# Performance work log

Hardware: AMD Instinct MI355X
Metric: run time of the kernel (lower is better)

## Reference

```python
import jax, jax.numpy as jnp
import numpy as np

N_NODES = 20000
N_EDGES = 640000
HIDDEN = 256
HEADS = 8
HEAD_DIM = HIDDEN // HEADS
VOCAB = 119
N_FEATS = 9


def setup_inputs() -> dict:
    key = jax.random.key(0)
    ks = jax.random.split(key, 12)
    X = jax.random.randint(ks[0], (N_NODES, N_FEATS), 0, VOCAB)
    edge_row = jnp.sort(jax.random.randint(ks[1], (N_EDGES,), 0, N_NODES))
    edge_col = jax.random.randint(ks[2], (N_EDGES,), 0, N_NODES)
    s = 0.05  # init scale to keep activations sane
    emb_tables = jax.random.normal(ks[3], (N_FEATS, VOCAB, HIDDEN), jnp.float32) * s
    q_w = jax.random.normal(ks[4], (HIDDEN, HIDDEN), jnp.float32) * s
    q_b = jax.random.normal(ks[5], (HIDDEN,), jnp.float32) * s
    k_w = jax.random.normal(ks[6], (HIDDEN, HIDDEN), jnp.float32) * s
    k_b = jax.random.normal(ks[7], (HIDDEN,), jnp.float32) * s
    v_w = jax.random.normal(ks[8], (HIDDEN, HIDDEN), jnp.float32) * s
    v_b = jax.random.normal(ks[9], (HIDDEN,), jnp.float32) * s
    o_w = jax.random.normal(ks[10], (HIDDEN, HIDDEN), jnp.float32) * s
    o_b = jax.random.normal(ks[11], (HIDDEN,), jnp.float32) * s
    return dict(X=X, edge_row=edge_row, edge_col=edge_col, emb_tables=emb_tables,
                q_w=q_w, q_b=q_b, k_w=k_w, k_b=k_b, v_w=v_w, v_b=v_b, o_w=o_w, o_b=o_b)


def reference(X, edge_row, edge_col, emb_tables, q_w, q_b, k_w, k_b, v_w, v_b, o_w, o_b):
    N = X.shape[0]
    # AtomEncoder: sum of per-feature embeddings -> [N, HIDDEN]
    feat_idx = jnp.arange(N_FEATS)[None, :]  # [1, 9]
    h = emb_tables[feat_idx, X].sum(axis=1)  # [N, 9, H] -> [N, H]
    # q/k/v projections (torch Linear: y = x W^T + b), split into heads
    q = (h @ q_w.T + q_b).reshape(N, HEADS, HEAD_DIM) * (HEAD_DIM ** -0.5)
    k = (h @ k_w.T + k_b).reshape(N, HEADS, HEAD_DIM)
    v = (h @ v_w.T + v_b).reshape(N, HEADS, HEAD_DIM)
    # SDDMM: per-edge, per-head scores
    s = jnp.einsum('ehd,ehd->eh', q[edge_row], k[edge_col])  # [E, HEADS]
    # sparse row-wise softmax (over each node's outgoing-edge neighbors)
    m = jax.ops.segment_max(s, edge_row, num_segments=N)
    e = jnp.exp(s - m[edge_row])
    z = jax.ops.segment_sum(e, edge_row, num_segments=N)
    attn = e / z[edge_row]  # [E, HEADS]
    # SPMM: weighted aggregation of neighbor values
    out = jax.ops.segment_sum(attn[:, :, None] * v[edge_col], edge_row, num_segments=N)
    return out.reshape(N, HIDDEN) @ o_w.T + o_b
```

## Files before the change

### kernel.cpp

```cpp
#include <hip/hip_runtime.h>
#include <hip/hip_bf16.h>

#define N_NODES 20000
#define N_EDGES 640000
#define HIDDEN 256
#define HEADS 8
#define HEAD_DIM 32
#define N_FEATS 9
#define VOCAB 119

typedef __hip_bfloat16 bf16;
typedef __attribute__((ext_vector_type(8))) short short8;
typedef __attribute__((ext_vector_type(4))) float f32x4;
typedef __attribute__((ext_vector_type(2))) float f32x2;

__device__ __forceinline__ ushort f2u(float x) { union { ushort u; bf16 b; } c; c.b = __float2bfloat16(x); return c.u; }

__device__ __forceinline__ f32x2 pk_fma(f32x2 a, f32x2 b, f32x2 c) {
    f32x2 d;
    asm("v_pk_fma_f32 %0, %1, %2, %3" : "=v"(d) : "v"(a), "v"(b), "v"(c));
    return d;
}
__device__ __forceinline__ f32x2 pk_add(f32x2 a, f32x2 b) {
    f32x2 d;
    asm("v_pk_add_f32 %0, %1, %2" : "=v"(d) : "v"(a), "v"(b));
    return d;
}

template <int CTRL>
__device__ __forceinline__ float dpp_xor(float v) {
    return __int_as_float(__builtin_amdgcn_update_dpp(
        0, __float_as_int(v), CTRL, 0xf, 0xf, true));
}

__device__ __forceinline__ float fast_exp2(float x) {
#if __has_builtin(__builtin_amdgcn_exp2f)
    return __builtin_amdgcn_exp2f(x);
#else
    return exp2f(x);
#endif
}

#if __has_builtin(__builtin_amdgcn_fdot2_f32_bf16)
typedef __attribute__((ext_vector_type(2))) __bf16 bf16x2_t;
__device__ __forceinline__ float dot2bf(uint a, uint b, float c) {
    return __builtin_amdgcn_fdot2_f32_bf16(__builtin_bit_cast(bf16x2_t, a),
                                           __builtin_bit_cast(bf16x2_t, b), c, false);
}
#else
__device__ __forceinline__ float dot2bf(uint a, uint b, float c) {
    return c + __uint_as_float(a << 16) * __uint_as_float(b << 16)
             + __uint_as_float(a & 0xffff0000u) * __uint_as_float(b & 0xffff0000u);
}
#endif

__global__ void k_pre(const int* __restrict__ X, const float* __restrict__ emb,
                      bf16* __restrict__ h,
                      const float* __restrict__ qw, const float* __restrict__ kw,
                      const float* __restrict__ vw, const float* __restrict__ ow,
                      const float* __restrict__ qb, const float* __restrict__ kb,
                      const float* __restrict__ vb,
                      bf16* __restrict__ wqkv, bf16* __restrict__ wo,
                      float* __restrict__ qkvb,
                      const int* __restrict__ erow, int* __restrict__ row_ptr) {
    int b = blockIdx.x;
    if (b < 5000) {
        int tid = b * 256 + threadIdx.x;
        int n = tid >> 6;
        int c4 = (tid & 63) * 4;
        float4 a = make_float4(0.f, 0.f, 0.f, 0.f);
#pragma unroll
        for (int f = 0; f < N_FEATS; ++f) {
            int idx = X[n * N_FEATS + f];
            float4 e = *(const float4*)(emb + ((size_t)(f * VOCAB + idx)) * HIDDEN + c4);
            a.x += e.x; a.y += e.y; a.z += e.z; a.w += e.w;
        }
        ushort4 o = make_ushort4(f2u(a.x), f2u(a.y), f2u(a.z), f2u(a.w));
        *(ushort4*)((ushort*)h + (size_t)n * HIDDEN + c4) = o;
    } else if (b < 6027) {
        int i = (b - 5000) * 256 + threadIdx.x;
        if (i < 196608) {
            const float* s = i < 65536 ? qw : i < 131072 ? kw : vw;
            wqkv[i] = __float2bfloat16(s[i & 65535]);
        } else if (i < 262144) {
            wo[i - 196608] = __float2bfloat16(ow[i - 196608]);
        } else if (i < 262912) {
            int j = i - 262144;
            const float* s = j < 256 ? qb : j < 512 ? kb : vb;
            qkvb[j] = s[j & 255];
        }
    } else {
        int n = (b - 6027) * 256 + threadIdx.x;
        if (n > N_NODES) return;
        int lo = 0, hi = N_EDGES;
        while (lo < hi) {
            int mid = (lo + hi) >> 1;
            if (erow[mid] < n) lo = mid + 1; else hi = mid;
        }
        row_ptr[n] = lo;
    }
}

template <int MODE, bool GUARD, int TM>
__device__ __forceinline__ void gemm_core(const bf16* __restrict__ A,
                                          const bf16* __restrict__ W,
                                          const float* __restrict__ bias,
                                          void* __restrict__ Y0, void* __restrict__ Y1,
                                          float s_q, int n0, int d0) {
    constexpr int RI = TM / 32;
    __shared__ short As[TM * 72];
    __shared__ short Bs[128 * 72];
    int t = threadIdx.x;
    int lane = t & 63, w = t >> 6;
    int wr = (w >> 1) * (TM / 2), wc = (w & 1) * 64;
    int lr = lane & 15, quad = lane >> 4;

    f32x4 acc[RI][4] = {};
    short8 ra[RI], rb[4];
    int srowA[RI], skoA[RI], srowB[4], skoB[4];
#pragma unroll
    for (int it = 0; it < RI; ++it) { int c = t + 256 * it; srowA[it] = c >> 3; skoA[it] = (c & 7) * 8; }
#pragma unroll
    for (int it = 0; it < 4; ++it) { int c = t + 256 * it; srowB[it] = c >> 3; skoB[it] = (c & 7) * 8; }

#pragma unroll
    for (int it = 0; it < RI; ++it) {
        int n = n0 + srowA[it];
        short8 av = {};
        if (!GUARD || n < N_NODES) av = *(const short8*)(A + (size_t)n * HIDDEN + skoA[it]);
        ra[it] = av;
    }
#pragma unroll
    for (int it = 0; it < 4; ++it)
        rb[it] = *(const short8*)(W + (size_t)(d0 + srowB[it]) * HIDDEN + skoB[it]);
#pragma unroll
    for (int it = 0; it < RI; ++it) *(short8*)(&As[srowA[it] * 72 + skoA[it]]) = ra[it];
#pragma unroll
    for (int it = 0; it < 4; ++it)  *(short8*)(&Bs[srowB[it] * 72 + skoB[it]]) = rb[it];
    __syncthreads();

    for (int k0 = 64; k0 < 256; k0 += 64) {
#pragma unroll
        for (int it = 0; it < RI; ++it) {
            int n = n0 + srowA[it];
            short8 av = {};
            if (!GUARD || n < N_NODES) av = *(const short8*)(A + (size_t)n * HIDDEN + k0 + skoA[it]);
            ra[it] = av;
        }
#pragma unroll
        for (int it = 0; it < 4; ++it)
            rb[it] = *(const short8*)(W + (size_t)(d0 + srowB[it]) * HIDDEN + k0 + skoB[it]);
        {
            short8 af[RI][2], bfr[4][2];
#pragma unroll
            for (int i = 0; i < RI; ++i)
#pragma unroll
                for (int kk = 0; kk < 2; ++kk)
                    af[i][kk] = *(short8*)(&As[(wr + i * 16 + lr) * 72 + kk * 32 + quad * 8]);
#pragma unroll
            for (int j = 0; j < 4; ++j)
#pragma unroll
                for (int kk = 0; kk < 2; ++kk)
                    bfr[j][kk] = *(short8*)(&Bs[(wc + j * 16 + lr) * 72 + kk * 32 + quad * 8]);
#pragma unroll
            for (int kk = 0; kk < 2; ++kk)
#pragma unroll
                for (int i = 0; i < RI; ++i)
#pragma unroll
                    for (int j = 0; j < 4; ++j)
                        acc[i][j] = __builtin_amdgcn_mfma_f32_16x16x32_bf16(
                            af[i][kk], bfr[j][kk], acc[i][j], 0, 0, 0);
        }
        __syncthreads();
#pragma unroll
        for (int it = 0; it < RI; ++it) *(short8*)(&As[srowA[it] * 72 + skoA[it]]) = ra[it];
#pragma unroll
        for (int it = 0; it < 4; ++it)  *(short8*)(&Bs[srowB[it] * 72 + skoB[it]]) = rb[it];
        __syncthreads();
    }
    {
        short8 af[RI][2], bfr[4][2];
#pragma unroll
        for (int i = 0; i < RI; ++i)
#pragma unroll
            for (int kk = 0; kk < 2; ++kk)
                af[i][kk] = *(short8*)(&As[(wr + i * 16 + lr) * 72 + kk * 32 + quad * 8]);
#pragma unroll
        for (int j = 0; j < 4; ++j)
#pragma unroll
            for (int kk = 0; kk < 2; ++kk)
                bfr[j][kk] = *(short8*)(&Bs[(wc + j * 16 + lr) * 72 + kk * 32 + quad * 8]);
#pragma unroll
        for (int kk = 0; kk < 2; ++kk)
#pragma unroll
            for (int i = 0; i < RI; ++i)
#pragma unroll
                for (int j = 0; j < 4; ++j)
                    acc[i][j] = __builtin_amdgcn_mfma_f32_16x16x32_bf16(
                        af[i][kk], bfr[j][kk], acc[i][j], 0, 0, 0);
    }

#pragma unroll
    for (int j = 0; j < 4; ++j) {
        int dbase = d0 + wc + j * 16;
        float bj = bias[dbase + lr];
        if constexpr (MODE == 0) {
            float sc = (dbase < 256) ? s_q : 1.f;
            ushort* dst; int stride;
            if (dbase < 256) {
                dst = (ushort*)Y0 + (size_t)(dbase >> 6) * N_NODES * 64 + (dbase & 63) + lr;
                stride = 64;
            } else if (dbase < 512) {
                int e = dbase - 256;
                dst = (ushort*)Y1 + (size_t)(e >> 6) * N_NODES * 128 + (e & 63) + lr;
                stride = 128;
            } else {
                int e = dbase - 512;
                dst = (ushort*)Y1 + (size_t)(e >> 6) * N_NODES * 128 + 64 + (e & 63) + lr;
                stride = 128;
            }
#pragma unroll
            for (int i = 0; i < RI; ++i)
#pragma unroll
                for (int r = 0; r < 4; ++r) {
                    int n = n0 + wr + i * 16 + quad * 4 + r;
                    if (GUARD && n >= N_NODES) continue;
                    dst[(size_t)n * stride] = f2u((acc[i][j][r] + bj) * sc);
                }
        } else {
            float* dst = (float*)Y0 + dbase + lr;
#pragma unroll
            for (int i = 0; i < RI; ++i)
#pragma unroll
                for (int r = 0; r < 4; ++r) {
                    int n = n0 + wr + i * 16 + quad * 4 + r;
                    if (GUARD && n >= N_NODES) continue;
                    dst[(size_t)n * HIDDEN] = acc[i][j][r] + bj;
                }
        }
    }
}

__global__ __launch_bounds__(256, 2) void k_gemm_qkv(
    const bf16* __restrict__ A, const bf16* __restrict__ wqkv,
    const float* __restrict__ qkvb, ushort* __restrict__ qhp,
    ushort* __restrict__ kvhp, float qscale) {
    int n0 = blockIdx.x * 128;
    if (n0 + 128 <= N_NODES)
        gemm_core<0, false, 128>(A, wqkv, qkvb, qhp, kvhp, qscale, n0, blockIdx.y * 128);
    else
        gemm_core<0, true, 128>(A, wqkv, qkvb, qhp, kvhp, qscale, n0, blockIdx.y * 128);
}

__global__ __launch_bounds__(256, 4) void k_gemm_o(
    const bf16* __restrict__ A, const bf16* __restrict__ W,
    const float* __restrict__ bias, float* __restrict__ Y) {
    int n0 = blockIdx.x * 64;
    if (n0 + 64 <= N_NODES)
        gemm_core<1, false, 64>(A, W, bias, Y, nullptr, 1.f, n0, blockIdx.y * 128);
    else
        gemm_core<1, true, 64>(A, W, bias, Y, nullptr, 1.f, n0, blockIdx.y * 128);
}


template <int NIT>
__device__ __forceinline__ void pv_accum(const uint4* vv, const float* pb,
                                         f32x2& av0, f32x2& av1, f32x2& av2v, f32x2& av3) {
#pragma unroll
    for (int it = 0; it < NIT; ++it) {
        f32x2 pp; pp.x = pb[it]; pp.y = pb[it];
        f32x2 vf0, vf1, vf2, vf3;
        vf0.x = __uint_as_float(vv[it].x << 16); vf0.y = __uint_as_float(vv[it].x & 0xffff0000u);
        vf1.x = __uint_as_float(vv[it].y << 16); vf1.y = __uint_as_float(vv[it].y & 0xffff0000u);
        vf2.x = __uint_as_float(vv[it].z << 16); vf2.y = __uint_as_float(vv[it].z & 0xffff0000u);
        vf3.x = __uint_as_float(vv[it].w << 16); vf3.y = __uint_as_float(vv[it].w & 0xffff0000u);
        av0  = pk_fma(vf0, pp, av0);
        av1  = pk_fma(vf1, pp, av1);
        av2v = pk_fma(vf2, pp, av2v);
        av3  = pk_fma(vf3, pp, av3);
    }
}

__device__ __forceinline__ void attn_combine(int lane, int d8, float z,
                                             f32x2 av0, f32x2 av1, f32x2 av2v, f32x2 av3,
                                             ushort* __restrict__ orow) {
    bool b3 = (lane & 8) != 0, b4 = (lane & 16) != 0, b5 = (lane & 32) != 0;
    f32x2 sd0 = b3 ? av0 : av2v;
    f32x2 sd1 = b3 ? av1 : av3;
    f32x2 r0, r1;
    r0.x = dpp_xor<0x128>(sd0.x); r0.y = dpp_xor<0x128>(sd0.y);
    r1.x = dpp_xor<0x128>(sd1.x); r1.y = dpp_xor<0x128>(sd1.y);
    f32x2 t0 = pk_add(b3 ? av2v : av0, r0);
    f32x2 t1 = pk_add(b3 ? av3  : av1, r1);
    f32x2 sdu = b4 ? t0 : t1;
    f32x2 ru; ru.x = __shfl_xor(sdu.x, 16); ru.y = __shfl_xor(sdu.y, 16);
    f32x2 u = pk_add(b4 ? t1 : t0, ru);
    float sw = b5 ? u.x : u.y;
    float rw = __shfl_xor(sw, 32);
    float w = (b5 ? u.y : u.x) + rw;
    int dim = d8 * 8 + ((lane >> 3) & 1) * 4 + ((lane >> 4) & 1) * 2 + ((lane >> 5) & 1);
    orow[dim] = f2u(w * (1.f / z));
}

__global__ __launch_bounds__(256, 4) void k_attn(
    const int* __restrict__ row_ptr, const int* __restrict__ col,
    const ushort* __restrict__ qhp, const ushort* __restrict__ kvhp,
    bf16* __restrict__ agg) {
    int b = blockIdx.x;
    int x = b & 7;
    int hp = x & 3;
    int wave = __builtin_amdgcn_readfirstlane((int)(threadIdx.x >> 6));
    int n = (b >> 3) * 8 + (x >> 2) * 4 + wave;
    int lane = threadIdx.x & 63;
    int my = lane >> 3;
    int d8 = lane & 7;

    int start = row_ptr[n];
    int deg = row_ptr[n + 1] - start;

    ushort* orow = (ushort*)agg + (size_t)n * HIDDEN + hp * 64;
    if (deg == 0) {
        if (lane < 8) { uint4 zo = {}; *(uint4*)(orow + lane * 8) = zo; }
        return;
    }

    const ushort* qrow = qhp + ((size_t)hp * N_NODES + n) * 64;
    const ushort* kvbase = kvhp + (size_t)hp * N_NODES * 128;
    const int* cb = col + start;

    if (deg <= 32) {
        int e = lane >> 1, h = lane & 1;
        int c_e = cb[min(e, deg - 1)];
        const ushort* kp = kvbase + (((size_t)(uint)c_e) << 7) + (uint)h * 32;
        const ushort* qp = qrow + (uint)h * 32;

        int cv[4]; uint4 vv[4];
#pragma unroll
        for (int it = 0; it < 4; ++it) cv[it] = __shfl(c_e, (it * 8 + my) * 2);
#pragma unroll
        for (int it = 0; it < 4; ++it)
            vv[it] = *(const uint4*)(kvbase + (((size_t)(uint)cv[it]) << 7) + 64 + (uint)d8 * 8);

        uint4 kk[4], qq[4];
#pragma unroll
        for (int i = 0; i < 4; ++i) kk[i] = *(const uint4*)(kp + i * 8);
#pragma unroll
        for (int i = 0; i < 4; ++i) qq[i] = *(const uint4*)(qp + i * 8);

        float c0 = dot2bf(kk[0].x, qq[0].x, 0.f);
        float c1 = dot2bf(kk[0].y, qq[0].y, 0.f);
        float c2 = dot2bf(kk[0].z, qq[0].z, 0.f);
        float c3 = dot2bf(kk[0].w, qq[0].w, 0.f);
#pragma unroll
        for (int i = 1; i < 4; ++i) {
            c0 = dot2bf(kk[i].x, qq[i].x, c0);
            c1 = dot2bf(kk[i].y, qq[i].y, c1);
            c2 = dot2bf(kk[i].z, qq[i].z, c2);
            c3 = dot2bf(kk[i].w, qq[i].w, c3);
        }
        float s = (c0 + c1) + (c2 + c3);
        float p = (e < deg) ? fast_exp2(s) : 0.f;

        float z = p;
        z += dpp_xor<0x4E>(z);
        z += dpp_xor<0x124>(z);
        z += dpp_xor<0x128>(z);
        z += __shfl_xor(z, 16);
        z += __shfl_xor(z, 32);
        float zo = __shfl_xor(z, 1);
        float zf = (h == (d8 >> 2)) ? z : zo;

        float pb[4];
#pragma unroll
        for (int it = 0; it < 4; ++it)
            pb[it] = __shfl(p, (it * 8 + my) * 2 + (d8 >> 2));

        f32x2 av0 = {0.f, 0.f}, av1 = {0.f, 0.f}, av2v = {0.f, 0.f}, av3 = {0.f, 0.f};
        pv_accum<4>(vv, pb, av0, av1, av2v, av3);
        attn_combine(lane, d8, zf, av0, av1, av2v, av3, orow);

    } else if (deg <= 64) {
        int c_all = cb[min(lane, deg - 1)];
        const ushort* kp = kvbase + (((size_t)(uint)c_all) << 7);

        int cv[8]; uint4 vv[8];
#pragma unroll
        for (int it = 0; it < 8; ++it) cv[it] = __shfl(c_all, it * 8 + my);
#pragma unroll
        for (int it = 0; it < 8; ++it)
            vv[it] = *(const uint4*)(kvbase + (((size_t)(uint)cv[it]) << 7) + 64 + (uint)d8 * 8);

        uint4 kk[8], qv[8];
#pragma unroll
        for (int i = 0; i < 8; ++i) kk[i] = *(const uint4*)(kp + i * 8);
#pragma unroll
        for (int i = 0; i < 8; ++i) qv[i] = *(const uint4*)(qrow + i * 8);

        float a0 = dot2bf(kk[0].x, qv[0].x, 0.f);
        float a1 = dot2bf(kk[0].y, qv[0].y, 0.f);
        float a2 = dot2bf(kk[0].z, qv[0].z, 0.f);
        float a3 = dot2bf(kk[0].w, qv[0].w, 0.f);
        float b0 = dot2bf(kk[4].x, qv[4].x, 0.f);
        float b1 = dot2bf(kk[4].y, qv[4].y, 0.f);
        float b2 = dot2bf(kk[4].z, qv[4].z, 0.f);
        float b3s = dot2bf(kk[4].w, qv[4].w, 0.f);
#pragma unroll
        for (int i = 1; i < 4; ++i) {
            a0 = dot2bf(kk[i].x, qv[i].x, a0);
            a1 = dot2bf(kk[i].y, qv[i].y, a1);
            a2 = dot2bf(kk[i].z, qv[i].z, a2);
            a3 = dot2bf(kk[i].w, qv[i].w, a3);
            b0 = dot2bf(kk[4 + i].x, qv[4 + i].x, b0);
            b1 = dot2bf(kk[4 + i].y, qv[4 + i].y, b1);
            b2 = dot2bf(kk[4 + i].z, qv[4 + i].z, b2);
            b3s = dot2bf(kk[4 + i].w, qv[4 + i].w, b3s);
        }
        float sA = (a0 + a1) + (a2 + a3);
        float sB = (b0 + b1) + (b2 + b3s);
        bool val = lane < deg;
        float pA = val ? fast_exp2(sA) : 0.f;
        float pB = val ? fast_exp2(sB) : 0.f;

        f32x2 zz; zz.x = pA; zz.y = pB;
        {
            f32x2 r;
            r.x = dpp_xor<0xB1>(zz.x);  r.y = dpp_xor<0xB1>(zz.y);  zz = pk_add(zz, r);
            r.x = dpp_xor<0x4E>(zz.x);  r.y = dpp_xor<0x4E>(zz.y);  zz = pk_add(zz, r);
            r.x = dpp_xor<0x124>(zz.x); r.y = dpp_xor<0x124>(zz.y); zz = pk_add(zz, r);
            r.x = dpp_xor<0x128>(zz.x); r.y = dpp_xor<0x128>(zz.y); zz = pk_add(zz, r);
            r.x = __shfl_xor(zz.x, 16); r.y = __shfl_xor(zz.y, 16); zz = pk_add(zz, r);
            r.x = __shfl_xor(zz.x, 32); r.y = __shfl_xor(zz.y, 32); zz = pk_add(zz, r);
        }
        float zf = (d8 < 4) ? zz.x : zz.y;

        bool hB = (d8 >= 4);
        float pb[8];
#pragma unroll
        for (int it = 0; it < 8; ++it) {
            float pa_ = __shfl(pA, it * 8 + my);
            float pb_ = __shfl(pB, it * 8 + my);
            pb[it] = hB ? pb_ : pa_;
        }

        f32x2 av0 = {0.f, 0.f}, av1 = {0.f, 0.f}, av2v = {0.f, 0.f}, av3 = {0.f, 0.f};
        pv_accum<8>(vv, pb, av0, av1, av2v, av3);
        attn_combine(lane, d8, zf, av0, av1, av2v, av3, orow);

    } else {
        uint4 qu = *(const uint4*)(qrow + d8 * 8);
        float z = 0.f;
        f32x2 av0 = {0.f, 0.f}, av1 = {0.f, 0.f}, av2v = {0.f, 0.f}, av3 = {0.f, 0.f};
        for (int i = 0; i < deg; i += 8) {
            int idx = i + my;
            int cidx = idx < deg ? idx : deg - 1;
            int c = cb[cidx];
            const ushort* kp = kvbase + (((size_t)(uint)c) << 7) + (uint)d8 * 8;
            uint4 ku = *(const uint4*)(kp);
            uint4 vu = *(const uint4*)(kp + 64);
            float s = dot2bf(ku.x, qu.x, 0.f);
            s = dot2bf(ku.y, qu.y, s);
            s = dot2bf(ku.z, qu.z, s);
            s = dot2bf(ku.w, qu.w, s);
            s += dpp_xor<0xB1>(s);
            s += dpp_xor<0x4E>(s);
            float p = (idx < deg) ? fast_exp2(s) : 0.f;
            z += p;
            f32x2 pp; pp.x = p; pp.y = p;
            f32x2 vf0, vf1, vf2, vf3;
            vf0.x = __uint_as_float(vu.x << 16); vf0.y = __uint_as_float(vu.x & 0xffff0000u);
            vf1.x = __uint_as_float(vu.y << 16); vf1.y = __uint_as_float(vu.y & 0xffff0000u);
            vf2.x = __uint_as_float(vu.z << 16); vf2.y = __uint_as_float(vu.z & 0xffff0000u);
            vf3.x = __uint_as_float(vu.w << 16); vf3.y = __uint_as_float(vu.w & 0xffff0000u);
            av0  = pk_fma(vf0, pp, av0);
            av1  = pk_fma(vf1, pp, av1);
            av2v = pk_fma(vf2, pp, av2v);
            av3  = pk_fma(vf3, pp, av3);
        }
        z += dpp_xor<0x128>(z);
        z += __shfl_xor(z, 16);
        z += __shfl_xor(z, 32);
        attn_combine(lane, d8, z, av0, av1, av2v, av3, orow);
    }
}

extern "C" void kernel_launch(void* const* d_in, const int* in_sizes, int n_in,
                              void* d_out, int out_size, void* d_ws, size_t ws_size,
                              hipStream_t stream) {
    const int*   X    = (const int*)d_in[0];
    const int*   erow = (const int*)d_in[1];
    const int*   ecol = (const int*)d_in[2];
    const float* emb  = (const float*)d_in[3];
    const float* q_w  = (const float*)d_in[4];
    const float* q_b  = (const float*)d_in[5];
    const float* k_w  = (const float*)d_in[6];
    const float* k_b  = (const float*)d_in[7];
    const float* v_w  = (const float*)d_in[8];
    const float* v_b  = (const float*)d_in[9];
    const float* o_w  = (const float*)d_in[10];
    const float* o_b  = (const float*)d_in[11];
    float* out = (float*)d_out;

    char* ws = (char*)d_ws;
    bf16*   h    = (bf16*)(ws);
    bf16*   agg  = (bf16*)(ws);
    ushort* qhp  = (ushort*)(ws + 10240000);
    ushort* kvhp = (ushort*)(ws + 20480000);
    bf16*   wqkv = (bf16*)(ws + 40960000);
    bf16*   wo   = (bf16*)(ws + 41353216);
    float*  qkvb = (float*)(ws + 41484288);
    int* row_ptr = (int*)(ws + 41487360);

    k_pre<<<6106, 256, 0, stream>>>(X, emb, h, q_w, k_w, v_w, o_w,
                                    q_b, k_b, v_b, wqkv, wo, qkvb, erow, row_ptr);

    const float qscale = 0.25503486121587466f;
    dim3 gqkv((N_NODES + 127) / 128, 768 / 128);
    k_gemm_qkv<<<gqkv, 256, 0, stream>>>(h, wqkv, qkvb, qhp, kvhp, qscale);

    k_attn<<<N_NODES, 256, 0, stream>>>(row_ptr, ecol, qhp, kvhp, agg);

    dim3 go((N_NODES + 63) / 64, HIDDEN / 128);
    k_gemm_o<<<go, 256, 0, stream>>>(agg, wo, o_b, out);
}
```

Measured before the change: 190.0 us.

## Unify small-degree attention paths into edge-per-8-lane layout with scheduling fence

Replaces the two small-degree branches (where one or two lanes computed a whole head-pair score from many strided K and Q loads) with a shared templated path. In it each group of 8 lanes owns one edge, each lane loads only one 16-byte K chunk, and a single Q chunk is reused across edges. Scores are reduced with DPP, so the later per-edge probability shuffles disappear and the softmax sum is taken per lane. A sched_barrier keeps all gather loads issued before any compute, which aims to improve memory-level parallelism and cut register use on Q loads. The cost is extra cross-lane reductions per edge and more rigid instruction scheduling.

```diff
diff --git a/kernel.cpp b/kernel.cpp
--- a/kernel.cpp
+++ b/kernel.cpp
@@ -39,6 +39,10 @@
 #else
     return exp2f(x);
 #endif
+}
+
+__device__ __forceinline__ void sched_fence() {
+    __builtin_amdgcn_sched_barrier(0);
 }
 
 #if __has_builtin(__builtin_amdgcn_fdot2_f32_bf16)
@@ -302,6 +306,54 @@
     orow[dim] = f2u(w * (1.f / z));
 }
 
+template <int NIT>
+__device__ __forceinline__ void attn_dense(const int* __restrict__ cb, int deg,
+                                           int lane, int my, int d8,
+                                           const ushort* __restrict__ qrow,
+                                           const ushort* __restrict__ kvbase,
+                                           ushort* __restrict__ orow) {
+    int degm8 = deg - my;
+    int c_all = cb[min(lane, deg - 1)];
+    uint d8b = (uint)d8 * 8;
+
+    int cc[NIT];
+#pragma unroll
+    for (int it = 0; it < NIT; ++it) cc[it] = __shfl(c_all, it * 8 + my);
+
+    uint4 qu = *(const uint4*)(qrow + d8b);
+    uint4 kk[NIT], vv[NIT];
+#pragma unroll
+    for (int it = 0; it < NIT; ++it)
+        kk[it] = *(const uint4*)(kvbase + (((size_t)(uint)cc[it]) << 7) + d8b);
+#pragma unroll
+    for (int it = 0; it < NIT; ++it)
+        vv[it] = *(const uint4*)(kvbase + (((size_t)(uint)cc[it]) << 7) + 64 + d8b);
+
+    sched_fence();
+
+    float z = 0.f;
+    float pb[NIT];
+#pragma unroll
+    for (int it = 0; it < NIT; ++it) {
+        float s = dot2bf(kk[it].x, qu.x, 0.f);
+        s = dot2bf(kk[it].y, qu.y, s);
+        s = dot2bf(kk[it].z, qu.z, s);
+        s = dot2bf(kk[it].w, qu.w, s);
+        s += dpp_xor<0xB1>(s);
+        s += dpp_xor<0x4E>(s);
+        float p = (it * 8 < degm8) ? fast_exp2(s) : 0.f;
+        z += p;
+        pb[it] = p;
+    }
+    z += dpp_xor<0x128>(z);
+    z += __shfl_xor(z, 16);
+    z += __shfl_xor(z, 32);
+
+    f32x2 av0 = {0.f, 0.f}, av1 = {0.f, 0.f}, av2v = {0.f, 0.f}, av3 = {0.f, 0.f};
+    pv_accum<NIT>(vv, pb, av0, av1, av2v, av3);
+    attn_combine(lane, d8, z, av0, av1, av2v, av3, orow);
+}
+
 __global__ __launch_bounds__(256, 4) void k_attn(
     const int* __restrict__ row_ptr, const int* __restrict__ col,
     const ushort* __restrict__ qhp, const ushort* __restrict__ kvhp,
@@ -329,123 +381,9 @@
     const int* cb = col + start;
 
     if (deg <= 32) {
-        int e = lane >> 1, h = lane & 1;
-        int c_e = cb[min(e, deg - 1)];
-        const ushort* kp = kvbase + (((size_t)(uint)c_e) << 7) + (uint)h * 32;
-        const ushort* qp = qrow + (uint)h * 32;
-
-        int cv[4]; uint4 vv[4];
-#pragma unroll
-        for (int it = 0; it < 4; ++it) cv[it] = __shfl(c_e, (it * 8 + my) * 2);
-#pragma unroll
-        for (int it = 0; it < 4; ++it)
-            vv[it] = *(const uint4*)(kvbase + (((size_t)(uint)cv[it]) << 7) + 64 + (uint)d8 * 8);
-
-        uint4 kk[4], qq[4];
-#pragma unroll
-        for (int i = 0; i < 4; ++i) kk[i] = *(const uint4*)(kp + i * 8);
-#pragma unroll
-        for (int i = 0; i < 4; ++i) qq[i] = *(const uint4*)(qp + i * 8);
-
-        float c0 = dot2bf(kk[0].x, qq[0].x, 0.f);
-        float c1 = dot2bf(kk[0].y, qq[0].y, 0.f);
-        float c2 = dot2bf(kk[0].z, qq[0].z, 0.f);
-        float c3 = dot2bf(kk[0].w, qq[0].w, 0.f);
-#pragma unroll
-        for (int i = 1; i < 4; ++i) {
-            c0 = dot2bf(kk[i].x, qq[i].x, c0);
-            c1 = dot2bf(kk[i].y, qq[i].y, c1);
-            c2 = dot2bf(kk[i].z, qq[i].z, c2);
-            c3 = dot2bf(kk[i].w, qq[i].w, c3);
-        }
-        float s = (c0 + c1) + (c2 + c3);
-        float p = (e < deg) ? fast_exp2(s) : 0.f;
-
-        float z = p;
-        z += dpp_xor<0x4E>(z);
-        z += dpp_xor<0x124>(z);
-        z += dpp_xor<0x128>(z);
-        z += __shfl_xor(z, 16);
-        z += __shfl_xor(z, 32);
-        float zo = __shfl_xor(z, 1);
-        float zf = (h == (d8 >> 2)) ? z : zo;
-
-        float pb[4];
-#pragma unroll
-        for (int it = 0; it < 4; ++it)
-            pb[it] = __shfl(p, (it * 8 + my) * 2 + (d8 >> 2));
-
-        f32x2 av0 = {0.f, 0.f}, av1 = {0.f, 0.f}, av2v = {0.f, 0.f}, av3 = {0.f, 0.f};
-        pv_accum<4>(vv, pb, av0, av1, av2v, av3);
-        attn_combine(lane, d8, zf, av0, av1, av2v, av3, orow);
-
+        attn_dense<4>(cb, deg, lane, my, d8, qrow, kvbase, orow);
     } else if (deg <= 64) {
-        int c_all = cb[min(lane, deg - 1)];
-        const ushort* kp = kvbase + (((size_t)(uint)c_all) << 7);
-
-        int cv[8]; uint4 vv[8];
-#pragma unroll
-        for (int it = 0; it < 8; ++it) cv[it] = __shfl(c_all, it * 8 + my);
-#pragma unroll
-        for (int it = 0; it < 8; ++it)
-            vv[it] = *(const uint4*)(kvbase + (((size_t)(uint)cv[it]) << 7) + 64 + (uint)d8 * 8);
-
-        uint4 kk[8], qv[8];
-#pragma unroll
-        for (int i = 0; i < 8; ++i) kk[i] = *(const uint4*)(kp + i * 8);
-#pragma unroll
-        for (int i = 0; i < 8; ++i) qv[i] = *(const uint4*)(qrow + i * 8);
-
-        float a0 = dot2bf(kk[0].x, qv[0].x, 0.f);
-        float a1 = dot2bf(kk[0].y, qv[0].y, 0.f);
-        float a2 = dot2bf(kk[0].z, qv[0].z, 0.f);
-        float a3 = dot2bf(kk[0].w, qv[0].w, 0.f);
-        float b0 = dot2bf(kk[4].x, qv[4].x, 0.f);
-        float b1 = dot2bf(kk[4].y, qv[4].y, 0.f);
-        float b2 = dot2bf(kk[4].z, qv[4].z, 0.f);
-        float b3s = dot2bf(kk[4].w, qv[4].w, 0.f);
-#pragma unroll
-        for (int i = 1; i < 4; ++i) {
-            a0 = dot2bf(kk[i].x, qv[i].x, a0);
-            a1 = dot2bf(kk[i].y, qv[i].y, a1);
-            a2 = dot2bf(kk[i].z, qv[i].z, a2);
-            a3 = dot2bf(kk[i].w, qv[i].w, a3);
-            b0 = dot2bf(kk[4 + i].x, qv[4 + i].x, b0);
-            b1 = dot2bf(kk[4 + i].y, qv[4 + i].y, b1);
-            b2 = dot2bf(kk[4 + i].z, qv[4 + i].z, b2);
-            b3s = dot2bf(kk[4 + i].w, qv[4 + i].w, b3s);
-        }
-        float sA = (a0 + a1) + (a2 + a3);
-        float sB = (b0 + b1) + (b2 + b3s);
-        bool val = lane < deg;
-        float pA = val ? fast_exp2(sA) : 0.f;
-        float pB = val ? fast_exp2(sB) : 0.f;
-
-        f32x2 zz; zz.x = pA; zz.y = pB;
-        {
-            f32x2 r;
-            r.x = dpp_xor<0xB1>(zz.x);  r.y = dpp_xor<0xB1>(zz.y);  zz = pk_add(zz, r);
-            r.x = dpp_xor<0x4E>(zz.x);  r.y = dpp_xor<0x4E>(zz.y);  zz = pk_add(zz, r);
-            r.x = dpp_xor<0x124>(zz.x); r.y = dpp_xor<0x124>(zz.y); zz = pk_add(zz, r);
-            r.x = dpp_xor<0x128>(zz.x); r.y = dpp_xor<0x128>(zz.y); zz = pk_add(zz, r);
-            r.x = __shfl_xor(zz.x, 16); r.y = __shfl_xor(zz.y, 16); zz = pk_add(zz, r);
-            r.x = __shfl_xor(zz.x, 32); r.y = __shfl_xor(zz.y, 32); zz = pk_add(zz, r);
-        }
-        float zf = (d8 < 4) ? zz.x : zz.y;
-
-        bool hB = (d8 >= 4);
-        float pb[8];
-#pragma unroll
-        for (int it = 0; it < 8; ++it) {
-            float pa_ = __shfl(pA, it * 8 + my);
-            float pb_ = __shfl(pB, it * 8 + my);
-            pb[it] = hB ? pb_ : pa_;
-        }
-
-        f32x2 av0 = {0.f, 0.f}, av1 = {0.f, 0.f}, av2v = {0.f, 0.f}, av3 = {0.f, 0.f};
-        pv_accum<8>(vv, pb, av0, av1, av2v, av3);
-        attn_combine(lane, d8, zf, av0, av1, av2v, av3, orow);
-
+        attn_dense<8>(cb, deg, lane, my, d8, qrow, kvbase, orow);
     } else {
         uint4 qu = *(const uint4*)(qrow + d8 * 8);
         float z = 0.f;
```

New measurement: 172.7 us. -9.1%, faster.
